# Performance work log

Measured on AMD Instinct MI355X. Metric: run time of the kernel, lower is better.

## Reference

```python
import jax, jax.numpy as jnp
import numpy as np

B, T, D = 2, 2048, 2048
NH, NKV, HD = 16, 4, 128
EPS = 1e-6
ROPE_THETA = 10000.0


def rms_norm(x, w):
    # per-head RMSNorm over the last (head_dim) axis
    var = jnp.mean(jnp.square(x), axis=-1, keepdims=True)
    return x * jax.lax.rsqrt(var + EPS) * w


def rope_sin_cos(seq_len, dim, dtype):
    inv_freq = 1.0 / (ROPE_THETA ** (jnp.arange(0, dim, 2, dtype=jnp.float32) / dim))
    t = jnp.arange(seq_len, dtype=jnp.float32)
    ang = jnp.outer(t, inv_freq)                      # [T, HD/2]
    ang = jnp.concatenate([ang, ang], axis=-1)         # [T, HD]
    return jnp.sin(ang).astype(dtype), jnp.cos(ang).astype(dtype)


def rotate_half(x):
    x1, x2 = jnp.split(x, 2, axis=-1)
    return jnp.concatenate([-x2, x1], axis=-1)


def apply_rope(x, sin, cos):
    # x: [B, T, H, HD]; sin/cos: [T, HD]
    s = sin[None, :, None, :]
    c = cos[None, :, None, :]
    return x * c + rotate_half(x) * s


def setup_inputs() -> dict:
    key = jax.random.key(0)
    ks = jax.random.split(key, 5)
    scale = 1.0 / np.sqrt(D)
    return {
        "x": jax.random.normal(ks[0], (B, T, D), jnp.float32),
        "wq": jax.random.normal(ks[1], (D, D), jnp.float32) * scale,
        "wk": jax.random.normal(ks[2], (NKV * HD, D), jnp.float32) * scale,
        "wv": jax.random.normal(ks[3], (NKV * HD, D), jnp.float32) * scale,
        "wo": jax.random.normal(ks[4], (D, D), jnp.float32) * scale,
        "q_norm_w": jnp.ones((HD,), jnp.float32),
        "k_norm_w": jnp.ones((HD,), jnp.float32),
    }


def reference(x, wq, wk, wv, wo, q_norm_w, k_norm_w):
    b, t, _ = x.shape
    q = (x @ wq.T).reshape(b, t, NH, HD)    # [B,T,NH,HD]
    k = (x @ wk.T).reshape(b, t, NKV, HD)   # [B,T,NKV,HD]
    v = (x @ wv.T).reshape(b, t, NKV, HD)

    # per-head QK RMS norm
    q = rms_norm(q, q_norm_w)
    k = rms_norm(k, k_norm_w)

    # RoPE
    sin, cos = rope_sin_cos(t, HD, x.dtype)
    q = apply_rope(q, sin, cos)
    k = apply_rope(k, sin, cos)

    # GQA: expand kv heads to match query heads
    rep = NH // NKV
    k = jnp.repeat(k, rep, axis=2)          # [B,T,NH,HD]
    v = jnp.repeat(v, rep, axis=2)

    # causal SDPA
    scale = 1.0 / np.sqrt(HD)
    scores = jnp.einsum('bqhd,bkhd->bhqk', q, k) * scale
    causal = jnp.tril(jnp.ones((t, t), bool))
    scores = jnp.where(causal[None, None], scores, jnp.finfo(scores.dtype).min)
    probs = jax.nn.softmax(scores, axis=-1)
    att = jnp.einsum('bhqk,bkhd->bqhd', probs, v).reshape(b, t, NH * HD)
    return att @ wo.T
```

## Files before the change

kernel.cpp:

```cpp
#include <hip/hip_runtime.h>
#include <hip/hip_bf16.h>

#define B_ 2
#define T_ 2048
#define D_ 2048
#define NH_ 16
#define NKV_ 4
#define HD_ 128

using bf16 = __bf16;
using bf16x8 = __attribute__((ext_vector_type(8))) __bf16;
using bf16x4 = __attribute__((ext_vector_type(4))) __bf16;
using f32x4 = __attribute__((ext_vector_type(4))) float;

__device__ __forceinline__ void gld_lds16(bf16* lds, const bf16* g) {
  __builtin_amdgcn_global_load_lds(
      (const __attribute__((address_space(1))) void*)g,
      (__attribute__((address_space(3))) void*)lds, 16, 0, 0);
}

__global__ __launch_bounds__(256) void cvt_all(const float* __restrict__ x,
                                               const float* __restrict__ wq,
                                               const float* __restrict__ wk,
                                               const float* __restrict__ wv,
                                               const float* __restrict__ wo,
                                               bf16* __restrict__ xb,
                                               bf16* __restrict__ wqkvb,
                                               bf16* __restrict__ wob) {
  const int bid = blockIdx.x;
  const float* src;
  bf16* dst;
  int base;
  if (bid < 8192)       { src = x;  dst = xb;              base = bid; }
  else if (bid < 12288) { src = wq; dst = wqkvb;           base = bid - 8192; }
  else if (bid < 13312) { src = wk; dst = wqkvb + 4194304; base = bid - 12288; }
  else if (bid < 14336) { src = wv; dst = wqkvb + 5242880; base = bid - 13312; }
  else                  { src = wo; dst = wob;             base = bid - 14336; }
  const int i = base * 256 + threadIdx.x;
  float4 v = ((const float4*)src)[i];
  bf16x4 o;
  o[0] = (bf16)v.x; o[1] = (bf16)v.y; o[2] = (bf16)v.z; o[3] = (bf16)v.w;
  ((bf16x4*)dst)[i] = o;
}

template<typename OutT>
__global__ __launch_bounds__(256) void gemm_bt(const bf16* __restrict__ A,
                                               const bf16* __restrict__ Bt,
                                               OutT* __restrict__ C,
                                               int M, int N, int K) {
  __shared__ bf16 As[3][128 * 32];
  __shared__ bf16 Bs[3][128 * 32];
  const int tid = threadIdx.x;
  const int wid = tid >> 6;
  const int lane = tid & 63;
  const int g = lane >> 4, r = lane & 15;
  const int wm = wid >> 1, wn = wid & 1;
  const int gx = gridDim.x;
  const int nwg = gx * gridDim.y;
  const int flat = blockIdx.y * gx + blockIdx.x;
  const int swz = (flat & 7) * (nwg >> 3) + (flat >> 3);
  const long bm = (long)(swz / gx) * 128, bn = (long)(swz % gx) * 128;
  f32x4 acc[4][4] = {};
  const int NT = K >> 5;

  auto stage = [&](int buf, int k0) {
    for (int c = 0; c < 2; ++c) {
      int ch = wid * 2 + c;
      int row = ch * 16 + (lane >> 2);
      int col = (lane & 3) * 8;
      gld_lds16(&As[buf][ch * 512], A + (bm + row) * K + k0 + col);
      gld_lds16(&Bs[buf][ch * 512], Bt + (bn + row) * K + k0 + col);
    }
  };

  stage(0, 0);
  stage(1, 32);
  for (int t = 0; t < NT; ++t) {
    if (t + 1 < NT)
      asm volatile("s_waitcnt vmcnt(4)" ::: "memory");
    else
      asm volatile("s_waitcnt vmcnt(0)" ::: "memory");
    __builtin_amdgcn_s_barrier();
    if (t + 2 < NT) stage((t + 2) % 3, (t + 2) * 32);
    const bf16* as = As[t % 3];
    const bf16* bs = Bs[t % 3];
    bf16x8 af[4], bfr[4];
    for (int m = 0; m < 4; ++m)
      af[m] = *(const bf16x8*)(as + (wm * 64 + m * 16 + r) * 32 + g * 8);
    for (int n = 0; n < 4; ++n)
      bfr[n] = *(const bf16x8*)(bs + (wn * 64 + n * 16 + r) * 32 + g * 8);
    for (int m = 0; m < 4; ++m)
      for (int n = 0; n < 4; ++n)
        acc[m][n] = __builtin_amdgcn_mfma_f32_16x16x32_bf16(af[m], bfr[n], acc[m][n], 0, 0, 0);
  }

  for (int m = 0; m < 4; ++m)
    for (int n = 0; n < 4; ++n)
      for (int e = 0; e < 4; ++e) {
        long row = bm + wm * 64 + m * 16 + g * 4 + e;
        long col = bn + wn * 64 + n * 16 + r;
        C[row * N + col] = (OutT)acc[m][n][e];
      }
}

__global__ __launch_bounds__(256) void prep_kv(const bf16* __restrict__ qkv,
                                               const float* __restrict__ kw,
                                               bf16* __restrict__ Kb,
                                               bf16* __restrict__ Vt) {
  __shared__ float tile[64][65];
  const int bid = blockIdx.x;
  if (bid < 4096) {
    const int lane = threadIdx.x & 63;
    const int rloc = threadIdx.x >> 6;
    const long rid = (long)bid * 4 + rloc;
    const int h = (int)(rid % NKV_);
    const long bt = rid / NKV_;
    const int t = (int)(bt % T_);
    const bf16* src = qkv + bt * 3072 + 2048 + h * HD_;
    float v0 = (float)src[lane];
    float v1 = (float)src[lane + 64];
    float ss = v0 * v0 + v1 * v1;
    for (int o = 1; o < 64; o <<= 1) ss += __shfl_xor(ss, o, 64);
    float inv = rsqrtf(ss * (1.f / HD_) + 1e-6f);
    float n0 = v0 * inv * kw[lane];
    float n1 = v1 * inv * kw[lane + 64];
    float ang = (float)t * exp2f((float)lane * (-13.287712379549449f / 64.f));
    float sv, cv;
    __sincosf(ang, &sv, &cv);
    long b = bt / T_;
    bf16* dst = Kb + ((b * NKV_ + h) * (long)T_ + t) * HD_;
    dst[lane] = (bf16)(n0 * cv - n1 * sv);
    dst[lane + 64] = (bf16)(n1 * cv + n0 * sv);
  } else {
    const int bid2 = bid - 4096;
    const int tt = bid2 & 31;
    const int by = bid2 >> 5;
    const int dd = by & 1;
    const int bkv = by >> 1;
    const long b = bkv >> 2;
    const int kv = bkv & 3;
    const int t0 = tt * 64, d0 = dd * 64;
    for (int i = 0; i < 2; ++i) {
      int row = i * 32 + (threadIdx.x >> 3);
      int c8 = (threadIdx.x & 7) * 8;
      bf16x8 v = *(const bf16x8*)&qkv[(b * T_ + t0 + row) * 3072 + 2560 + kv * HD_ + d0 + c8];
      for (int j = 0; j < 8; ++j) tile[row][c8 + j] = (float)v[j];
    }
    __syncthreads();
    for (int i = 0; i < 2; ++i) {
      int drow = i * 32 + (threadIdx.x >> 3);
      int tc8 = (threadIdx.x & 7) * 8;
      bf16x8 o;
      for (int j = 0; j < 8; ++j) o[j] = (bf16)tile[tc8 + j][drow];
      *(bf16x8*)&Vt[((b * NKV_ + kv) * (long)HD_ + d0 + drow) * T_ + t0 + tc8] = o;
    }
  }
}

__global__ __launch_bounds__(512) void flash_attn(const bf16* __restrict__ QKV,
                                                  const float* __restrict__ qw,
                                                  const bf16* __restrict__ K,
                                                  const bf16* __restrict__ V,
                                                  bf16* __restrict__ O) {
  __shared__ bf16 Ks[2][64 * 128];
  __shared__ bf16 Vs[2][128 * 64];
  __shared__ bf16 Ps[8][16 * 64];
  const int h = blockIdx.y, b = blockIdx.z;
  const int qt = b ? blockIdx.x : (gridDim.x - 1) - blockIdx.x;
  const int kv = h >> 2;
  const int tid = threadIdx.x, wid = tid >> 6, lane = tid & 63;
  const int g = lane >> 4, r = lane & 15;
  const int q0 = qt * 128;
  const int qbase = q0 + wid * 16;
  const int q = qbase + r;

  const bf16* qsrc = QKV + ((long)(b * T_ + q)) * 3072 + h * HD_;
  float ss = 0.f;
  for (int kk = 0; kk < 4; ++kk) {
    bf16x8 tq = *(const bf16x8*)(qsrc + kk * 32 + g * 8);
    for (int j = 0; j < 8; ++j) { float f = (float)tq[j]; ss += f * f; }
  }
  ss += __shfl_xor(ss, 16, 64);
  ss += __shfl_xor(ss, 32, 64);
  const float inv = rsqrtf(ss * (1.f / HD_) + 1e-6f);
  bf16x8 aq[4];
  for (int kk = 0; kk < 2; ++kk) {
    bf16x8 tlo = *(const bf16x8*)(qsrc + kk * 32 + g * 8);
    bf16x8 thi = *(const bf16x8*)(qsrc + kk * 32 + 64 + g * 8);
    bf16x8 alo, ahi;
    for (int j = 0; j < 8; ++j) {
      const int d = kk * 32 + g * 8 + j;
      float n0 = (float)tlo[j] * inv * qw[d];
      float n1 = (float)thi[j] * inv * qw[d + 64];
      float ang = (float)q * exp2f((float)d * (-13.287712379549449f / 64.f));
      float sv, cv;
      __sincosf(ang, &sv, &cv);
      alo[j] = (bf16)(n0 * cv - n1 * sv);
      ahi[j] = (bf16)(n1 * cv + n0 * sv);
    }
    aq[kk] = alo;
    aq[kk + 2] = ahi;
  }

  f32x4 oacc[8] = {};
  float m_run = -1e30f, l_run = 0.f;

  const bf16* Kbase = K + ((long)(b * NKV_ + kv)) * T_ * HD_;
  const bf16* Vbase = V + ((long)(b * NKV_ + kv)) * (long)HD_ * T_;
  const int nkt = 2 * qt + 2;

  auto stageKV = [&](int buf, int k0) {
    for (int c = 0; c < 2; ++c) {
      int ch = wid * 2 + c;
      {
        int row = ch * 4 + (lane >> 4);
        int srccol = ((lane & 15) ^ (row & 7)) * 8;
        gld_lds16(&Ks[buf][ch * 512], Kbase + (long)(k0 + row) * HD_ + srccol);
      }
      {
        int row = ch * 8 + (lane >> 3);
        int srccol = ((lane & 7) ^ (row & 7)) * 8;
        gld_lds16(&Vs[buf][ch * 512], Vbase + (long)row * T_ + k0 + srccol);
      }
    }
  };

  stageKV(0, 0);
  for (int kt = 0; kt < nkt; ++kt) {
    const int k0 = kt * 64;
    const int cur = kt & 1;
    if (kt + 1 < nkt) {
      stageKV(cur ^ 1, k0 + 64);
      asm volatile("s_waitcnt vmcnt(4)" ::: "memory");
    } else {
      asm volatile("s_waitcnt vmcnt(0)" ::: "memory");
    }
    __builtin_amdgcn_s_barrier();

    f32x4 s[4] = {};
    __builtin_amdgcn_s_setprio(1);
    for (int n = 0; n < 4; ++n)
      for (int kk = 0; kk < 4; ++kk) {
        int row = n * 16 + r;
        bf16x8 bk = *(const bf16x8*)(&Ks[cur][row * 128 + (((kk * 4 + g) ^ (row & 7)) * 8)]);
        s[n] = __builtin_amdgcn_mfma_f32_16x16x32_bf16(bk, aq[kk], s[n], 0, 0, 0);
      }
    __builtin_amdgcn_s_setprio(0);

    const float scale = 0.088388347648318447f;
    const bool domask = (k0 + 63 > qbase);
    float mx = -1e30f;
    if (domask) {
      for (int n = 0; n < 4; ++n) {
        const int km = k0 + n * 16 + g * 4;
        for (int e = 0; e < 4; ++e) {
          float v = s[n][e] * scale;
          if (km + e > q) v = -1e30f;
          s[n][e] = v;
          mx = fmaxf(mx, v);
        }
      }
    } else {
      for (int n = 0; n < 4; ++n)
        for (int e = 0; e < 4; ++e) {
          float v = s[n][e] * scale;
          s[n][e] = v;
          mx = fmaxf(mx, v);
        }
    }
    mx = fmaxf(mx, __shfl_xor(mx, 16, 64));
    mx = fmaxf(mx, __shfl_xor(mx, 32, 64));
    float mnew = fmaxf(m_run, mx);
    float alpha = __expf(m_run - mnew);
    float ls = 0.f;
    for (int n = 0; n < 4; ++n) {
      bf16x4 pb;
      for (int e = 0; e < 4; ++e) {
        float p = __expf(s[n][e] - mnew);
        ls += p;
        pb[e] = (bf16)p;
      }
      int c = n * 2 + (g >> 1);
      *(bf16x4*)(&Ps[wid][r * 64 + ((c ^ (r & 7)) * 8) + (g & 1) * 4]) = pb;
    }
    ls += __shfl_xor(ls, 16, 64);
    ls += __shfl_xor(ls, 32, 64);
    m_run = mnew;
    l_run = l_run * alpha + ls;

    float al[4];
    for (int e = 0; e < 4; ++e)
      al[e] = __shfl(alpha, (lane & 48) | (g * 4 + e), 64);
    for (int dt = 0; dt < 8; ++dt)
      for (int e = 0; e < 4; ++e) oacc[dt][e] *= al[e];

    asm volatile("s_waitcnt lgkmcnt(0)" ::: "memory");

    __builtin_amdgcn_s_setprio(1);
    for (int kk = 0; kk < 2; ++kk) {
      bf16x8 ap = *(const bf16x8*)(&Ps[wid][r * 64 + (((kk * 4 + g) ^ (r & 7)) * 8)]);
      for (int dt = 0; dt < 8; ++dt) {
        int row = dt * 16 + r;
        bf16x8 bv = *(const bf16x8*)(&Vs[cur][row * 64 + (((kk * 4 + g) ^ (row & 7)) * 8)]);
        oacc[dt] = __builtin_amdgcn_mfma_f32_16x16x32_bf16(ap, bv, oacc[dt], 0, 0, 0);
      }
    }
    __builtin_amdgcn_s_setprio(0);
    __builtin_amdgcn_s_barrier();
  }

  float li[4];
  for (int e = 0; e < 4; ++e) {
    float lv = __shfl(l_run, (lane & 48) | (g * 4 + e), 64);
    li[e] = 1.f / lv;
  }
  for (int e = 0; e < 4; ++e) {
    const int grow = q0 + wid * 16 + g * 4 + e;
    bf16* dst = O + ((long)(b * T_ + grow)) * (NH_ * HD_) + h * HD_;
    for (int dt = 0; dt < 8; ++dt)
      dst[dt * 16 + r] = (bf16)(oacc[dt][e] * li[e]);
  }
}

extern "C" void kernel_launch(void* const* d_in, const int* in_sizes, int n_in,
                              void* d_out, int out_size, void* d_ws, size_t ws_size,
                              hipStream_t stream) {
  const float* x  = (const float*)d_in[0];
  const float* wq = (const float*)d_in[1];
  const float* wk = (const float*)d_in[2];
  const float* wv = (const float*)d_in[3];
  const float* wo = (const float*)d_in[4];
  const float* qw = (const float*)d_in[5];
  const float* kw = (const float*)d_in[6];
  float* out = (float*)d_out;

  char* p = (char*)d_ws;
  bf16* xb    = (bf16*)(p);
  bf16* wqkvb = (bf16*)(p + 16777216);
  bf16* wob   = (bf16*)(p + 29360128);
  bf16* QKVr  = (bf16*)(p + 37748736);
  bf16* Kb    = (bf16*)(p + 79691776);
  bf16* Vt    = (bf16*)(p + 83886080);
  bf16* attb  = (bf16*)(p + 88080384);

  cvt_all<<<18432, 256, 0, stream>>>(x, wq, wk, wv, wo, xb, wqkvb, wob);

  gemm_bt<bf16><<<dim3(24, 32), 256, 0, stream>>>(xb, wqkvb, QKVr, 4096, 3072, 2048);

  prep_kv<<<4608, 256, 0, stream>>>(QKVr, kw, Kb, Vt);

  flash_attn<<<dim3(16, 16, 2), 512, 0, stream>>>(QKVr, qw, Kb, Vt, attb);

  gemm_bt<float><<<dim3(16, 32), 256, 0, stream>>>(attb, wob, out, 4096, 2048, 2048);
}
```

Measured before the change: 207.2 us.

## Balance causal flash attention work by splitting long query tiles across blocks

Each block now gets an equal amount of causal work. The first 8 bins process the first 17 key tiles of a long query tile. The other bins process the remainder of one long query tile plus a whole short query tile. Partial outputs of the long tiles are written as unnormalized bf16 values along with their running max and sum, and a new merge kernel combines the two pieces. This removes the tail imbalance of the causal triangle. The cost is an extra kernel launch, partial writes and reads in bf16, and reuse of the workspace region that held xb.

```diff
diff --git a/kernel.cpp b/kernel.cpp
--- a/kernel.cpp
+++ b/kernel.cpp
@@ -161,53 +161,32 @@
                                                   const float* __restrict__ qw,
                                                   const bf16* __restrict__ K,
                                                   const bf16* __restrict__ V,
-                                                  bf16* __restrict__ O) {
+                                                  bf16* __restrict__ O,
+                                                  bf16* __restrict__ OPart,
+                                                  float* __restrict__ Mst,
+                                                  float* __restrict__ Lst) {
   __shared__ bf16 Ks[2][64 * 128];
   __shared__ bf16 Vs[2][128 * 64];
   __shared__ bf16 Ps[8][16 * 64];
+  const int bin = blockIdx.x;
   const int h = blockIdx.y, b = blockIdx.z;
-  const int qt = b ? blockIdx.x : (gridDim.x - 1) - blockIdx.x;
   const int kv = h >> 2;
   const int tid = threadIdx.x, wid = tid >> 6, lane = tid & 63;
   const int g = lane >> 4, r = lane & 15;
-  const int q0 = qt * 128;
-  const int qbase = q0 + wid * 16;
-  const int q = qbase + r;
-
-  const bf16* qsrc = QKV + ((long)(b * T_ + q)) * 3072 + h * HD_;
-  float ss = 0.f;
-  for (int kk = 0; kk < 4; ++kk) {
-    bf16x8 tq = *(const bf16x8*)(qsrc + kk * 32 + g * 8);
-    for (int j = 0; j < 8; ++j) { float f = (float)tq[j]; ss += f * f; }
+
+  int segQt[2], segBeg[2], segEnd[2], nseg;
+  if (bin < 8) {
+    nseg = 1;
+    segQt[0] = 15 - bin; segBeg[0] = 0; segEnd[0] = 17;
+  } else {
+    const int i = bin - 8;
+    nseg = 2;
+    segQt[0] = 15 - i; segBeg[0] = 17; segEnd[0] = 2 * (15 - i) + 2;
+    segQt[1] = i;      segBeg[1] = 0;  segEnd[1] = 2 * i + 2;
   }
-  ss += __shfl_xor(ss, 16, 64);
-  ss += __shfl_xor(ss, 32, 64);
-  const float inv = rsqrtf(ss * (1.f / HD_) + 1e-6f);
-  bf16x8 aq[4];
-  for (int kk = 0; kk < 2; ++kk) {
-    bf16x8 tlo = *(const bf16x8*)(qsrc + kk * 32 + g * 8);
-    bf16x8 thi = *(const bf16x8*)(qsrc + kk * 32 + 64 + g * 8);
-    bf16x8 alo, ahi;
-    for (int j = 0; j < 8; ++j) {
-      const int d = kk * 32 + g * 8 + j;
-      float n0 = (float)tlo[j] * inv * qw[d];
-      float n1 = (float)thi[j] * inv * qw[d + 64];
-      float ang = (float)q * exp2f((float)d * (-13.287712379549449f / 64.f));
-      float sv, cv;
-      __sincosf(ang, &sv, &cv);
-      alo[j] = (bf16)(n0 * cv - n1 * sv);
-      ahi[j] = (bf16)(n1 * cv + n0 * sv);
-    }
-    aq[kk] = alo;
-    aq[kk + 2] = ahi;
-  }
-
-  f32x4 oacc[8] = {};
-  float m_run = -1e30f, l_run = 0.f;
 
   const bf16* Kbase = K + ((long)(b * NKV_ + kv)) * T_ * HD_;
   const bf16* Vbase = V + ((long)(b * NKV_ + kv)) * (long)HD_ * T_;
-  const int nkt = 2 * qt + 2;
 
   auto stageKV = [&](int buf, int k0) {
     for (int c = 0; c < 2; ++c) {
@@ -225,101 +204,188 @@
     }
   };
 
-  stageKV(0, 0);
-  for (int kt = 0; kt < nkt; ++kt) {
-    const int k0 = kt * 64;
-    const int cur = kt & 1;
-    if (kt + 1 < nkt) {
-      stageKV(cur ^ 1, k0 + 64);
-      asm volatile("s_waitcnt vmcnt(4)" ::: "memory");
+  stageKV(0, segBeg[0] * 64);
+  int flat = 0;
+  for (int sg = 0; sg < nseg; ++sg) {
+    const int qt = segQt[sg];
+    const int q0 = qt * 128;
+    const int qbase = q0 + wid * 16;
+    const int q = qbase + r;
+
+    const bf16* qsrc = QKV + ((long)(b * T_ + q)) * 3072 + h * HD_;
+    float ssq = 0.f;
+    for (int kk = 0; kk < 4; ++kk) {
+      bf16x8 tq = *(const bf16x8*)(qsrc + kk * 32 + g * 8);
+      for (int j = 0; j < 8; ++j) { float f = (float)tq[j]; ssq += f * f; }
+    }
+    ssq += __shfl_xor(ssq, 16, 64);
+    ssq += __shfl_xor(ssq, 32, 64);
+    const float qinv = rsqrtf(ssq * (1.f / HD_) + 1e-6f);
+    bf16x8 aq[4];
+    for (int kk = 0; kk < 2; ++kk) {
+      bf16x8 tlo = *(const bf16x8*)(qsrc + kk * 32 + g * 8);
+      bf16x8 thi = *(const bf16x8*)(qsrc + kk * 32 + 64 + g * 8);
+      bf16x8 alo, ahi;
+      for (int j = 0; j < 8; ++j) {
+        const int d = kk * 32 + g * 8 + j;
+        float n0 = (float)tlo[j] * qinv * qw[d];
+        float n1 = (float)thi[j] * qinv * qw[d + 64];
+        float ang = (float)q * exp2f((float)d * (-13.287712379549449f / 64.f));
+        float sv, cv;
+        __sincosf(ang, &sv, &cv);
+        alo[j] = (bf16)(n0 * cv - n1 * sv);
+        ahi[j] = (bf16)(n1 * cv + n0 * sv);
+      }
+      aq[kk] = alo;
+      aq[kk + 2] = ahi;
+    }
+
+    f32x4 oacc[8] = {};
+    float m_run = -1e30f, l_run = 0.f;
+
+    const int kBeg = segBeg[sg], kEnd = segEnd[sg];
+    for (int kt = kBeg; kt < kEnd; ++kt, ++flat) {
+      const int k0 = kt * 64;
+      const int cur = flat & 1;
+      int k0n = -1;
+      if (kt + 1 < kEnd) k0n = (kt + 1) * 64;
+      else if (sg + 1 < nseg) k0n = segBeg[sg + 1] * 64;
+      if (k0n >= 0) {
+        stageKV(cur ^ 1, k0n);
+        asm volatile("s_waitcnt vmcnt(4)" ::: "memory");
+      } else {
+        asm volatile("s_waitcnt vmcnt(0)" ::: "memory");
+      }
+      __builtin_amdgcn_s_barrier();
+
+      f32x4 s[4] = {};
+      __builtin_amdgcn_s_setprio(1);
+      for (int n = 0; n < 4; ++n)
+        for (int kk = 0; kk < 4; ++kk) {
+          int row = n * 16 + r;
+          bf16x8 bk = *(const bf16x8*)(&Ks[cur][row * 128 + (((kk * 4 + g) ^ (row & 7)) * 8)]);
+          s[n] = __builtin_amdgcn_mfma_f32_16x16x32_bf16(bk, aq[kk], s[n], 0, 0, 0);
+        }
+      __builtin_amdgcn_s_setprio(0);
+
+      const float scale = 0.088388347648318447f;
+      const bool domask = (k0 + 63 > qbase);
+      float mx = -1e30f;
+      if (domask) {
+        for (int n = 0; n < 4; ++n) {
+          const int km = k0 + n * 16 + g * 4;
+          for (int e = 0; e < 4; ++e) {
+            float v = s[n][e] * scale;
+            if (km + e > q) v = -1e30f;
+            s[n][e] = v;
+            mx = fmaxf(mx, v);
+          }
+        }
+      } else {
+        for (int n = 0; n < 4; ++n)
+          for (int e = 0; e < 4; ++e) {
+            float v = s[n][e] * scale;
+            s[n][e] = v;
+            mx = fmaxf(mx, v);
+          }
+      }
+      mx = fmaxf(mx, __shfl_xor(mx, 16, 64));
+      mx = fmaxf(mx, __shfl_xor(mx, 32, 64));
+      float mnew = fmaxf(m_run, mx);
+      float alpha = __expf(m_run - mnew);
+      const float mden = fmaxf(mnew, -1e28f);
+      float ls = 0.f;
+      for (int n = 0; n < 4; ++n) {
+        bf16x4 pb;
+        for (int e = 0; e < 4; ++e) {
+          float p = __expf(s[n][e] - mden);
+          ls += p;
+          pb[e] = (bf16)p;
+        }
+        int c = n * 2 + (g >> 1);
+        *(bf16x4*)(&Ps[wid][r * 64 + ((c ^ (r & 7)) * 8) + (g & 1) * 4]) = pb;
+      }
+      ls += __shfl_xor(ls, 16, 64);
+      ls += __shfl_xor(ls, 32, 64);
+      m_run = mnew;
+      l_run = l_run * alpha + ls;
+
+      float al[4];
+      for (int e = 0; e < 4; ++e)
+        al[e] = __shfl(alpha, (lane & 48) | (g * 4 + e), 64);
+      for (int dt = 0; dt < 8; ++dt)
+        for (int e = 0; e < 4; ++e) oacc[dt][e] *= al[e];
+
+      asm volatile("s_waitcnt lgkmcnt(0)" ::: "memory");
+
+      __builtin_amdgcn_s_setprio(1);
+      for (int kk = 0; kk < 2; ++kk) {
+        bf16x8 ap = *(const bf16x8*)(&Ps[wid][r * 64 + (((kk * 4 + g) ^ (r & 7)) * 8)]);
+        for (int dt = 0; dt < 8; ++dt) {
+          int row = dt * 16 + r;
+          bf16x8 bv = *(const bf16x8*)(&Vs[cur][row * 64 + (((kk * 4 + g) ^ (row & 7)) * 8)]);
+          oacc[dt] = __builtin_amdgcn_mfma_f32_16x16x32_bf16(ap, bv, oacc[dt], 0, 0, 0);
+        }
+      }
+      __builtin_amdgcn_s_setprio(0);
+      __builtin_amdgcn_s_barrier();
+    }
+
+    if (qt >= 8) {
+      const int piece = (bin >= 8 && sg == 0) ? 1 : 0;
+      const int pid = (((b * 16 + h) * 8) + (qt - 8)) * 2 + piece;
+      bf16* dst0 = OPart + (long)pid * 16384;
+      for (int e = 0; e < 4; ++e) {
+        const int rowl = wid * 16 + g * 4 + e;
+        bf16* dst = dst0 + rowl * 128;
+        for (int dt = 0; dt < 8; ++dt) dst[dt * 16 + r] = (bf16)oacc[dt][e];
+      }
+      if (g == 0) {
+        Mst[pid * 128 + wid * 16 + r] = m_run;
+        Lst[pid * 128 + wid * 16 + r] = l_run;
+      }
     } else {
-      asm volatile("s_waitcnt vmcnt(0)" ::: "memory");
-    }
-    __builtin_amdgcn_s_barrier();
-
-    f32x4 s[4] = {};
-    __builtin_amdgcn_s_setprio(1);
-    for (int n = 0; n < 4; ++n)
-      for (int kk = 0; kk < 4; ++kk) {
-        int row = n * 16 + r;
-        bf16x8 bk = *(const bf16x8*)(&Ks[cur][row * 128 + (((kk * 4 + g) ^ (row & 7)) * 8)]);
-        s[n] = __builtin_amdgcn_mfma_f32_16x16x32_bf16(bk, aq[kk], s[n], 0, 0, 0);
-      }
-    __builtin_amdgcn_s_setprio(0);
-
-    const float scale = 0.088388347648318447f;
-    const bool domask = (k0 + 63 > qbase);
-    float mx = -1e30f;
-    if (domask) {
-      for (int n = 0; n < 4; ++n) {
-        const int km = k0 + n * 16 + g * 4;
-        for (int e = 0; e < 4; ++e) {
-          float v = s[n][e] * scale;
-          if (km + e > q) v = -1e30f;
-          s[n][e] = v;
-          mx = fmaxf(mx, v);
-        }
-      }
-    } else {
-      for (int n = 0; n < 4; ++n)
-        for (int e = 0; e < 4; ++e) {
-          float v = s[n][e] * scale;
-          s[n][e] = v;
-          mx = fmaxf(mx, v);
-        }
-    }
-    mx = fmaxf(mx, __shfl_xor(mx, 16, 64));
-    mx = fmaxf(mx, __shfl_xor(mx, 32, 64));
-    float mnew = fmaxf(m_run, mx);
-    float alpha = __expf(m_run - mnew);
-    float ls = 0.f;
-    for (int n = 0; n < 4; ++n) {
-      bf16x4 pb;
+      float li[4];
       for (int e = 0; e < 4; ++e) {
-        float p = __expf(s[n][e] - mnew);
-        ls += p;
-        pb[e] = (bf16)p;
-      }
-      int c = n * 2 + (g >> 1);
-      *(bf16x4*)(&Ps[wid][r * 64 + ((c ^ (r & 7)) * 8) + (g & 1) * 4]) = pb;
-    }
-    ls += __shfl_xor(ls, 16, 64);
-    ls += __shfl_xor(ls, 32, 64);
-    m_run = mnew;
-    l_run = l_run * alpha + ls;
-
-    float al[4];
-    for (int e = 0; e < 4; ++e)
-      al[e] = __shfl(alpha, (lane & 48) | (g * 4 + e), 64);
-    for (int dt = 0; dt < 8; ++dt)
-      for (int e = 0; e < 4; ++e) oacc[dt][e] *= al[e];
-
-    asm volatile("s_waitcnt lgkmcnt(0)" ::: "memory");
-
-    __builtin_amdgcn_s_setprio(1);
-    for (int kk = 0; kk < 2; ++kk) {
-      bf16x8 ap = *(const bf16x8*)(&Ps[wid][r * 64 + (((kk * 4 + g) ^ (r & 7)) * 8)]);
-      for (int dt = 0; dt < 8; ++dt) {
-        int row = dt * 16 + r;
-        bf16x8 bv = *(const bf16x8*)(&Vs[cur][row * 64 + (((kk * 4 + g) ^ (row & 7)) * 8)]);
-        oacc[dt] = __builtin_amdgcn_mfma_f32_16x16x32_bf16(ap, bv, oacc[dt], 0, 0, 0);
-      }
-    }
-    __builtin_amdgcn_s_setprio(0);
-    __builtin_amdgcn_s_barrier();
+        float lv = __shfl(l_run, (lane & 48) | (g * 4 + e), 64);
+        li[e] = 1.f / lv;
+      }
+      for (int e = 0; e < 4; ++e) {
+        const int grow = q0 + wid * 16 + g * 4 + e;
+        bf16* dst = O + ((long)(b * T_ + grow)) * (NH_ * HD_) + h * HD_;
+        for (int dt = 0; dt < 8; ++dt)
+          dst[dt * 16 + r] = (bf16)(oacc[dt][e] * li[e]);
+      }
+    }
   }
-
-  float li[4];
-  for (int e = 0; e < 4; ++e) {
-    float lv = __shfl(l_run, (lane & 48) | (g * 4 + e), 64);
-    li[e] = 1.f / lv;
-  }
-  for (int e = 0; e < 4; ++e) {
-    const int grow = q0 + wid * 16 + g * 4 + e;
-    bf16* dst = O + ((long)(b * T_ + grow)) * (NH_ * HD_) + h * HD_;
-    for (int dt = 0; dt < 8; ++dt)
-      dst[dt * 16 + r] = (bf16)(oacc[dt][e] * li[e]);
-  }
+}
+
+__global__ __launch_bounds__(256) void merge_o(const bf16* __restrict__ OPart,
+                                               const float* __restrict__ Mst,
+                                               const float* __restrict__ Lst,
+                                               bf16* __restrict__ attb) {
+  const int bid = blockIdx.x;
+  const int qi = bid >> 3;
+  const int row = (bid & 7) * 16 + (threadIdx.x >> 4);
+  const int d8 = (threadIdx.x & 15) * 8;
+  const int qt = 8 + (qi & 7);
+  const int hb = qi >> 3;
+  const int h = hb & 15;
+  const int b = hb >> 4;
+  const int pid0 = qi * 2;
+  const bf16* o0p = OPart + (long)pid0 * 16384 + row * 128 + d8;
+  const bf16* o1p = OPart + (long)(pid0 + 1) * 16384 + row * 128 + d8;
+  bf16x8 o0 = *(const bf16x8*)o0p;
+  bf16x8 o1 = *(const bf16x8*)o1p;
+  const float m0 = Mst[pid0 * 128 + row], l0 = Lst[pid0 * 128 + row];
+  const float m1 = Mst[(pid0 + 1) * 128 + row], l1 = Lst[(pid0 + 1) * 128 + row];
+  const float M = fmaxf(m0, m1);
+  const float w0 = __expf(m0 - M), w1 = __expf(m1 - M);
+  const float inv = 1.f / (l0 * w0 + l1 * w1);
+  bf16x8 res;
+  for (int j = 0; j < 8; ++j)
+    res[j] = (bf16)(((float)o0[j] * w0 + (float)o1[j] * w1) * inv);
+  *(bf16x8*)&attb[((long)(b * T_ + qt * 128 + row)) * 2048 + h * 128 + d8] = res;
 }
 
 extern "C" void kernel_launch(void* const* d_in, const int* in_sizes, int n_in,
@@ -342,6 +408,9 @@
   bf16* Kb    = (bf16*)(p + 79691776);
   bf16* Vt    = (bf16*)(p + 83886080);
   bf16* attb  = (bf16*)(p + 88080384);
+  bf16*  OPart = (bf16*)(p);
+  float* Mst   = (float*)(p + 16777216);
+  float* Lst   = (float*)(p + 17039360);
 
   cvt_all<<<18432, 256, 0, stream>>>(x, wq, wk, wv, wo, xb, wqkvb, wob);
 
@@ -349,7 +418,9 @@
 
   prep_kv<<<4608, 256, 0, stream>>>(QKVr, kw, Kb, Vt);
 
-  flash_attn<<<dim3(16, 16, 2), 512, 0, stream>>>(QKVr, qw, Kb, Vt, attb);
+  flash_attn<<<dim3(16, 16, 2), 512, 0, stream>>>(QKVr, qw, Kb, Vt, attb,
+                                                  OPart, Mst, Lst);
+  merge_o<<<2048, 256, 0, stream>>>(OPart, Mst, Lst, attb);
 
   gemm_bt<float><<<dim3(16, 32), 256, 0, stream>>>(attb, wob, out, 4096, 2048, 2048);
 }
```

Result: slower. 219.7 us (+6.0%).

## Split flash-attention key tiles across warp pairs with 64-row query blocks and merge

Applied to the files above, without the earlier changes.

Query tiles shrink from 128 to 64 rows and the grid doubles. Each pair of warps now splits every 64-key tile into two 32-key halves, keeping separate online-softmax states that are merged through shared memory at the end. The K/V double buffer becomes a single buffer, with the next tile's load issued only after the trailing barrier, which cuts LDS use to 40 KB so more blocks can be resident. The aim is more parallelism and better load balance across CUs, at the cost of losing the overlap between loads and compute, an extra merge step, and a clamp on the exp reference for fully masked rows.

```diff
diff --git a/kernel.cpp b/kernel.cpp
--- a/kernel.cpp
+++ b/kernel.cpp
@@ -162,27 +162,36 @@
                                                   const bf16* __restrict__ K,
                                                   const bf16* __restrict__ V,
                                                   bf16* __restrict__ O) {
-  __shared__ bf16 Ks[2][64 * 128];
-  __shared__ bf16 Vs[2][128 * 64];
-  __shared__ bf16 Ps[8][16 * 64];
+  __shared__ char smem[40960];
+  bf16* Ks = (bf16*)smem;
+  bf16* Vs = (bf16*)(smem + 16384);
+  bf16* Ps = (bf16*)(smem + 32768);
+  float* mergeO = (float*)smem;
+  float* mergeML = (float*)(smem + 32768);
+
   const int h = blockIdx.y, b = blockIdx.z;
-  const int qt = b ? blockIdx.x : (gridDim.x - 1) - blockIdx.x;
+  const int x = blockIdx.x;
+  const int y8 = (h >> 3) & 1;
+  const int qt = b ? (y8 ? 31 - (x ^ 1) : (x ^ 1)) : (y8 ? x : 31 - x);
   const int kv = h >> 2;
   const int tid = threadIdx.x, wid = tid >> 6, lane = tid & 63;
   const int g = lane >> 4, r = lane & 15;
-  const int q0 = qt * 128;
-  const int qbase = q0 + wid * 16;
+  const int f = wid >> 1;
+  const int gr = wid & 1;
+  const int ko = gr * 32;
+  const int q0 = qt * 64;
+  const int qbase = q0 + f * 16;
   const int q = qbase + r;
 
   const bf16* qsrc = QKV + ((long)(b * T_ + q)) * 3072 + h * HD_;
-  float ss = 0.f;
+  float ssq = 0.f;
   for (int kk = 0; kk < 4; ++kk) {
     bf16x8 tq = *(const bf16x8*)(qsrc + kk * 32 + g * 8);
-    for (int j = 0; j < 8; ++j) { float f = (float)tq[j]; ss += f * f; }
-  }
-  ss += __shfl_xor(ss, 16, 64);
-  ss += __shfl_xor(ss, 32, 64);
-  const float inv = rsqrtf(ss * (1.f / HD_) + 1e-6f);
+    for (int j = 0; j < 8; ++j) { float ff = (float)tq[j]; ssq += ff * ff; }
+  }
+  ssq += __shfl_xor(ssq, 16, 64);
+  ssq += __shfl_xor(ssq, 32, 64);
+  const float qinv = rsqrtf(ssq * (1.f / HD_) + 1e-6f);
   bf16x8 aq[4];
   for (int kk = 0; kk < 2; ++kk) {
     bf16x8 tlo = *(const bf16x8*)(qsrc + kk * 32 + g * 8);
@@ -190,8 +199,8 @@
     bf16x8 alo, ahi;
     for (int j = 0; j < 8; ++j) {
       const int d = kk * 32 + g * 8 + j;
-      float n0 = (float)tlo[j] * inv * qw[d];
-      float n1 = (float)thi[j] * inv * qw[d + 64];
+      float n0 = (float)tlo[j] * qinv * qw[d];
+      float n1 = (float)thi[j] * qinv * qw[d + 64];
       float ang = (float)q * exp2f((float)d * (-13.287712379549449f / 64.f));
       float sv, cv;
       __sincosf(ang, &sv, &cv);
@@ -207,52 +216,48 @@
 
   const bf16* Kbase = K + ((long)(b * NKV_ + kv)) * T_ * HD_;
   const bf16* Vbase = V + ((long)(b * NKV_ + kv)) * (long)HD_ * T_;
-  const int nkt = 2 * qt + 2;
-
-  auto stageKV = [&](int buf, int k0) {
+  const int nkt = qt + 1;
+
+  auto stageKV = [&](int k0) {
     for (int c = 0; c < 2; ++c) {
       int ch = wid * 2 + c;
       {
         int row = ch * 4 + (lane >> 4);
         int srccol = ((lane & 15) ^ (row & 7)) * 8;
-        gld_lds16(&Ks[buf][ch * 512], Kbase + (long)(k0 + row) * HD_ + srccol);
+        gld_lds16(&Ks[ch * 512], Kbase + (long)(k0 + row) * HD_ + srccol);
       }
       {
         int row = ch * 8 + (lane >> 3);
         int srccol = ((lane & 7) ^ (row & 7)) * 8;
-        gld_lds16(&Vs[buf][ch * 512], Vbase + (long)row * T_ + k0 + srccol);
+        gld_lds16(&Vs[ch * 512], Vbase + (long)row * T_ + k0 + srccol);
       }
     }
   };
 
-  stageKV(0, 0);
+  const float scale = 0.088388347648318447f;
+  bf16* myPs = Ps + wid * 512;
+
+  stageKV(0);
   for (int kt = 0; kt < nkt; ++kt) {
     const int k0 = kt * 64;
-    const int cur = kt & 1;
-    if (kt + 1 < nkt) {
-      stageKV(cur ^ 1, k0 + 64);
-      asm volatile("s_waitcnt vmcnt(4)" ::: "memory");
-    } else {
-      asm volatile("s_waitcnt vmcnt(0)" ::: "memory");
-    }
+    asm volatile("s_waitcnt vmcnt(0)" ::: "memory");
     __builtin_amdgcn_s_barrier();
 
-    f32x4 s[4] = {};
+    f32x4 s[2] = {};
     __builtin_amdgcn_s_setprio(1);
-    for (int n = 0; n < 4; ++n)
+    for (int n = 0; n < 2; ++n)
       for (int kk = 0; kk < 4; ++kk) {
-        int row = n * 16 + r;
-        bf16x8 bk = *(const bf16x8*)(&Ks[cur][row * 128 + (((kk * 4 + g) ^ (row & 7)) * 8)]);
+        int row = ko + n * 16 + r;
+        bf16x8 bk = *(const bf16x8*)(&Ks[row * 128 + (((kk * 4 + g) ^ (row & 7)) * 8)]);
         s[n] = __builtin_amdgcn_mfma_f32_16x16x32_bf16(bk, aq[kk], s[n], 0, 0, 0);
       }
     __builtin_amdgcn_s_setprio(0);
 
-    const float scale = 0.088388347648318447f;
-    const bool domask = (k0 + 63 > qbase);
+    const bool domask = (k0 + ko + 31 > qbase);
     float mx = -1e30f;
     if (domask) {
-      for (int n = 0; n < 4; ++n) {
-        const int km = k0 + n * 16 + g * 4;
+      for (int n = 0; n < 2; ++n) {
+        const int km = k0 + ko + n * 16 + g * 4;
         for (int e = 0; e < 4; ++e) {
           float v = s[n][e] * scale;
           if (km + e > q) v = -1e30f;
@@ -261,7 +266,7 @@
         }
       }
     } else {
-      for (int n = 0; n < 4; ++n)
+      for (int n = 0; n < 2; ++n)
         for (int e = 0; e < 4; ++e) {
           float v = s[n][e] * scale;
           s[n][e] = v;
@@ -272,16 +277,17 @@
     mx = fmaxf(mx, __shfl_xor(mx, 32, 64));
     float mnew = fmaxf(m_run, mx);
     float alpha = __expf(m_run - mnew);
+    const float mden = fmaxf(mnew, -1e28f);
     float ls = 0.f;
-    for (int n = 0; n < 4; ++n) {
+    for (int n = 0; n < 2; ++n) {
       bf16x4 pb;
       for (int e = 0; e < 4; ++e) {
-        float p = __expf(s[n][e] - mnew);
+        float p = __expf(s[n][e] - mden);
         ls += p;
         pb[e] = (bf16)p;
       }
       int c = n * 2 + (g >> 1);
-      *(bf16x4*)(&Ps[wid][r * 64 + ((c ^ (r & 7)) * 8) + (g & 1) * 4]) = pb;
+      *(bf16x4*)(&myPs[r * 32 + ((c ^ (r & 3)) * 8) + (g & 1) * 4]) = pb;
     }
     ls += __shfl_xor(ls, 16, 64);
     ls += __shfl_xor(ls, 32, 64);
@@ -297,28 +303,53 @@
     asm volatile("s_waitcnt lgkmcnt(0)" ::: "memory");
 
     __builtin_amdgcn_s_setprio(1);
-    for (int kk = 0; kk < 2; ++kk) {
-      bf16x8 ap = *(const bf16x8*)(&Ps[wid][r * 64 + (((kk * 4 + g) ^ (r & 7)) * 8)]);
+    {
+      bf16x8 ap = *(const bf16x8*)(&myPs[r * 32 + ((g ^ (r & 3)) * 8)]);
       for (int dt = 0; dt < 8; ++dt) {
         int row = dt * 16 + r;
-        bf16x8 bv = *(const bf16x8*)(&Vs[cur][row * 64 + (((kk * 4 + g) ^ (row & 7)) * 8)]);
+        bf16x8 bv = *(const bf16x8*)(&Vs[row * 64 + (((gr * 4 + g) ^ (row & 7)) * 8)]);
         oacc[dt] = __builtin_amdgcn_mfma_f32_16x16x32_bf16(ap, bv, oacc[dt], 0, 0, 0);
       }
     }
     __builtin_amdgcn_s_setprio(0);
     __builtin_amdgcn_s_barrier();
-  }
-
-  float li[4];
-  for (int e = 0; e < 4; ++e) {
-    float lv = __shfl(l_run, (lane & 48) | (g * 4 + e), 64);
-    li[e] = 1.f / lv;
-  }
-  for (int e = 0; e < 4; ++e) {
-    const int grow = q0 + wid * 16 + g * 4 + e;
-    bf16* dst = O + ((long)(b * T_ + grow)) * (NH_ * HD_) + h * HD_;
-    for (int dt = 0; dt < 8; ++dt)
-      dst[dt * 16 + r] = (bf16)(oacc[dt][e] * li[e]);
+    if (kt + 1 < nkt) stageKV(k0 + 64);
+  }
+
+  if (gr == 1) {
+    float* mo = mergeO + f * 2048;
+    for (int e = 0; e < 4; ++e)
+      for (int dt = 0; dt < 8; ++dt)
+        mo[(g * 4 + e) * 128 + dt * 16 + r] = oacc[dt][e];
+    if (g == 0) {
+      mergeML[f * 32 + r] = m_run;
+      mergeML[f * 32 + 16 + r] = l_run;
+    }
+  }
+  __syncthreads();
+  if (gr == 0) {
+    const float* mo = mergeO + f * 2048;
+    const float m1 = mergeML[f * 32 + r];
+    const float l1 = mergeML[f * 32 + 16 + r];
+    const float M = fmaxf(m_run, m1);
+    const float w0 = __expf(m_run - M);
+    const float w1 = __expf(m1 - M);
+    const float lt = l_run * w0 + l1 * w1;
+    float W0[4], W1[4], LI[4];
+    for (int e = 0; e < 4; ++e) {
+      const int src = (lane & 48) | (g * 4 + e);
+      W0[e] = __shfl(w0, src, 64);
+      W1[e] = __shfl(w1, src, 64);
+      LI[e] = 1.f / __shfl(lt, src, 64);
+    }
+    for (int e = 0; e < 4; ++e) {
+      const int grow = qbase + g * 4 + e;
+      bf16* dst = O + ((long)(b * T_ + grow)) * (NH_ * HD_) + h * HD_;
+      for (int dt = 0; dt < 8; ++dt) {
+        float o1 = mo[(g * 4 + e) * 128 + dt * 16 + r];
+        dst[dt * 16 + r] = (bf16)((oacc[dt][e] * W0[e] + o1 * W1[e]) * LI[e]);
+      }
+    }
   }
 }
 
@@ -349,7 +380,7 @@
 
   prep_kv<<<4608, 256, 0, stream>>>(QKVr, kw, Kb, Vt);
 
-  flash_attn<<<dim3(16, 16, 2), 512, 0, stream>>>(QKVr, qw, Kb, Vt, attb);
+  flash_attn<<<dim3(32, 16, 2), 512, 0, stream>>>(QKVr, qw, Kb, Vt, attb);
 
   gemm_bt<float><<<dim3(16, 32), 256, 0, stream>>>(attb, wob, out, 4096, 2048, 2048);
 }
```

Measured after the change: 237.0 us. 14.4% more time.

## Switch flash attention to 32x32x16 MFMA with register-resident P and 4 waves

Applied to the files above, without the earlier changes.

Rewrites the attention inner loop to use 32x32x16 bf16 MFMA tiles, with each wave owning 32 query rows, and halves the block to 256 threads. Softmax probabilities now stay in registers and are rearranged through a cross-half lane shuffle, so the shared-memory P buffer and its LDS round-trip go away. The per-row alpha and l broadcasts become lane-local, and output stores are vectorized. The cost is higher register pressure from the 16-wide accumulators and fewer waves per block for hiding latency.

```diff
diff --git a/kernel.cpp b/kernel.cpp
--- a/kernel.cpp
+++ b/kernel.cpp
@@ -12,6 +12,8 @@
 using bf16x8 = __attribute__((ext_vector_type(8))) __bf16;
 using bf16x4 = __attribute__((ext_vector_type(4))) __bf16;
 using f32x4 = __attribute__((ext_vector_type(4))) float;
+using f32x16 = __attribute__((ext_vector_type(16))) float;
+using u32x4 = __attribute__((ext_vector_type(4))) unsigned int;
 
 __device__ __forceinline__ void gld_lds16(bf16* lds, const bf16* g) {
   __builtin_amdgcn_global_load_lds(
@@ -157,52 +159,54 @@
   }
 }
 
-__global__ __launch_bounds__(512) void flash_attn(const bf16* __restrict__ QKV,
+__global__ __launch_bounds__(256) void flash_attn(const bf16* __restrict__ QKV,
                                                   const float* __restrict__ qw,
                                                   const bf16* __restrict__ K,
                                                   const bf16* __restrict__ V,
                                                   bf16* __restrict__ O) {
   __shared__ bf16 Ks[2][64 * 128];
   __shared__ bf16 Vs[2][128 * 64];
-  __shared__ bf16 Ps[8][16 * 64];
   const int h = blockIdx.y, b = blockIdx.z;
   const int qt = b ? blockIdx.x : (gridDim.x - 1) - blockIdx.x;
   const int kv = h >> 2;
   const int tid = threadIdx.x, wid = tid >> 6, lane = tid & 63;
-  const int g = lane >> 4, r = lane & 15;
+  const int ql = lane & 31, hi = lane >> 5;
   const int q0 = qt * 128;
-  const int qbase = q0 + wid * 16;
-  const int q = qbase + r;
-
-  const bf16* qsrc = QKV + ((long)(b * T_ + q)) * 3072 + h * HD_;
+  const int qbase = q0 + wid * 32;
+  const int qrow = qbase + ql;
+
+  const bf16* qsrc = QKV + ((long)(b * T_ + qrow)) * 3072 + h * HD_;
   float ss = 0.f;
-  for (int kk = 0; kk < 4; ++kk) {
-    bf16x8 tq = *(const bf16x8*)(qsrc + kk * 32 + g * 8);
+#pragma unroll
+  for (int t = 0; t < 8; ++t) {
+    bf16x8 tq = *(const bf16x8*)(qsrc + t * 16 + hi * 8);
+#pragma unroll
     for (int j = 0; j < 8; ++j) { float f = (float)tq[j]; ss += f * f; }
   }
-  ss += __shfl_xor(ss, 16, 64);
   ss += __shfl_xor(ss, 32, 64);
   const float inv = rsqrtf(ss * (1.f / HD_) + 1e-6f);
-  bf16x8 aq[4];
-  for (int kk = 0; kk < 2; ++kk) {
-    bf16x8 tlo = *(const bf16x8*)(qsrc + kk * 32 + g * 8);
-    bf16x8 thi = *(const bf16x8*)(qsrc + kk * 32 + 64 + g * 8);
+  bf16x8 aq[8];
+#pragma unroll
+  for (int t = 0; t < 4; ++t) {
+    bf16x8 tlo = *(const bf16x8*)(qsrc + t * 16 + hi * 8);
+    bf16x8 thi = *(const bf16x8*)(qsrc + (t + 4) * 16 + hi * 8);
     bf16x8 alo, ahi;
+#pragma unroll
     for (int j = 0; j < 8; ++j) {
-      const int d = kk * 32 + g * 8 + j;
+      const int d = t * 16 + hi * 8 + j;
       float n0 = (float)tlo[j] * inv * qw[d];
       float n1 = (float)thi[j] * inv * qw[d + 64];
-      float ang = (float)q * exp2f((float)d * (-13.287712379549449f / 64.f));
+      float ang = (float)qrow * exp2f((float)d * (-13.287712379549449f / 64.f));
       float sv, cv;
       __sincosf(ang, &sv, &cv);
       alo[j] = (bf16)(n0 * cv - n1 * sv);
       ahi[j] = (bf16)(n1 * cv + n0 * sv);
     }
-    aq[kk] = alo;
-    aq[kk + 2] = ahi;
-  }
-
-  f32x4 oacc[8] = {};
+    aq[t] = alo;
+    aq[t + 4] = ahi;
+  }
+
+  f32x16 oacc[4] = {};
   float m_run = -1e30f, l_run = 0.f;
 
   const bf16* Kbase = K + ((long)(b * NKV_ + kv)) * T_ * HD_;
@@ -210,8 +214,9 @@
   const int nkt = 2 * qt + 2;
 
   auto stageKV = [&](int buf, int k0) {
-    for (int c = 0; c < 2; ++c) {
-      int ch = wid * 2 + c;
+#pragma unroll
+    for (int c = 0; c < 4; ++c) {
+      int ch = wid * 4 + c;
       {
         int row = ch * 4 + (lane >> 4);
         int srccol = ((lane & 15) ^ (row & 7)) * 8;
@@ -224,6 +229,8 @@
       }
     }
   };
+
+  const float scale = 0.088388347648318447f;
 
   stageKV(0, 0);
   for (int kt = 0; kt < nkt; ++kt) {
@@ -231,95 +238,101 @@
     const int cur = kt & 1;
     if (kt + 1 < nkt) {
       stageKV(cur ^ 1, k0 + 64);
-      asm volatile("s_waitcnt vmcnt(4)" ::: "memory");
+      asm volatile("s_waitcnt vmcnt(8)" ::: "memory");
     } else {
       asm volatile("s_waitcnt vmcnt(0)" ::: "memory");
     }
     __builtin_amdgcn_s_barrier();
 
-    f32x4 s[4] = {};
+    f32x16 s[2] = {};
     __builtin_amdgcn_s_setprio(1);
-    for (int n = 0; n < 4; ++n)
-      for (int kk = 0; kk < 4; ++kk) {
-        int row = n * 16 + r;
-        bf16x8 bk = *(const bf16x8*)(&Ks[cur][row * 128 + (((kk * 4 + g) ^ (row & 7)) * 8)]);
-        s[n] = __builtin_amdgcn_mfma_f32_16x16x32_bf16(bk, aq[kk], s[n], 0, 0, 0);
-      }
+#pragma unroll
+    for (int kc = 0; kc < 2; ++kc) {
+      const int row = kc * 32 + ql;
+#pragma unroll
+      for (int t = 0; t < 8; ++t) {
+        bf16x8 bk = *(const bf16x8*)(&Ks[cur][row * 128 + (((2 * t + hi) ^ (row & 7)) * 8)]);
+        s[kc] = __builtin_amdgcn_mfma_f32_32x32x16_bf16(bk, aq[t], s[kc], 0, 0, 0);
+      }
+    }
     __builtin_amdgcn_s_setprio(0);
 
-    const float scale = 0.088388347648318447f;
     const bool domask = (k0 + 63 > qbase);
     float mx = -1e30f;
-    if (domask) {
-      for (int n = 0; n < 4; ++n) {
-        const int km = k0 + n * 16 + g * 4;
-        for (int e = 0; e < 4; ++e) {
-          float v = s[n][e] * scale;
-          if (km + e > q) v = -1e30f;
-          s[n][e] = v;
-          mx = fmaxf(mx, v);
+#pragma unroll
+    for (int kc = 0; kc < 2; ++kc)
+#pragma unroll
+      for (int r = 0; r < 16; ++r) {
+        float v = s[kc][r] * scale;
+        if (domask) {
+          int kg = k0 + kc * 32 + (r & 3) + 8 * (r >> 2) + 4 * hi;
+          if (kg > qrow) v = -1e30f;
         }
-      }
-    } else {
-      for (int n = 0; n < 4; ++n)
-        for (int e = 0; e < 4; ++e) {
-          float v = s[n][e] * scale;
-          s[n][e] = v;
-          mx = fmaxf(mx, v);
-        }
-    }
-    mx = fmaxf(mx, __shfl_xor(mx, 16, 64));
+        s[kc][r] = v;
+        mx = fmaxf(mx, v);
+      }
     mx = fmaxf(mx, __shfl_xor(mx, 32, 64));
-    float mnew = fmaxf(m_run, mx);
-    float alpha = __expf(m_run - mnew);
+    const float mnew = fmaxf(m_run, mx);
+    const float alpha = __expf(m_run - mnew);
     float ls = 0.f;
-    for (int n = 0; n < 4; ++n) {
-      bf16x4 pb;
-      for (int e = 0; e < 4; ++e) {
-        float p = __expf(s[n][e] - mnew);
-        ls += p;
-        pb[e] = (bf16)p;
-      }
-      int c = n * 2 + (g >> 1);
-      *(bf16x4*)(&Ps[wid][r * 64 + ((c ^ (r & 7)) * 8) + (g & 1) * 4]) = pb;
-    }
-    ls += __shfl_xor(ls, 16, 64);
+    unsigned int w[2][8];
+#pragma unroll
+    for (int kc = 0; kc < 2; ++kc)
+#pragma unroll
+      for (int i = 0; i < 8; ++i) {
+        float p0 = __expf(s[kc][2 * i] - mnew);
+        float p1 = __expf(s[kc][2 * i + 1] - mnew);
+        ls += p0 + p1;
+        unsigned short b0 = __builtin_bit_cast(unsigned short, (bf16)p0);
+        unsigned short b1 = __builtin_bit_cast(unsigned short, (bf16)p1);
+        w[kc][i] = ((unsigned int)b1 << 16) | (unsigned int)b0;
+      }
     ls += __shfl_xor(ls, 32, 64);
     m_run = mnew;
     l_run = l_run * alpha + ls;
-
-    float al[4];
-    for (int e = 0; e < 4; ++e)
-      al[e] = __shfl(alpha, (lane & 48) | (g * 4 + e), 64);
-    for (int dt = 0; dt < 8; ++dt)
-      for (int e = 0; e < 4; ++e) oacc[dt][e] *= al[e];
-
-    asm volatile("s_waitcnt lgkmcnt(0)" ::: "memory");
+#pragma unroll
+    for (int dt = 0; dt < 4; ++dt)
+#pragma unroll
+      for (int r = 0; r < 16; ++r) oacc[dt][r] *= alpha;
+
+    unsigned int xw[2][8];
+#pragma unroll
+    for (int kc = 0; kc < 2; ++kc)
+#pragma unroll
+      for (int i = 0; i < 8; ++i) xw[kc][i] = __shfl_xor(w[kc][i], 32, 64);
 
     __builtin_amdgcn_s_setprio(1);
-    for (int kk = 0; kk < 2; ++kk) {
-      bf16x8 ap = *(const bf16x8*)(&Ps[wid][r * 64 + (((kk * 4 + g) ^ (r & 7)) * 8)]);
-      for (int dt = 0; dt < 8; ++dt) {
-        int row = dt * 16 + r;
-        bf16x8 bv = *(const bf16x8*)(&Vs[cur][row * 64 + (((kk * 4 + g) ^ (row & 7)) * 8)]);
-        oacc[dt] = __builtin_amdgcn_mfma_f32_16x16x32_bf16(ap, bv, oacc[dt], 0, 0, 0);
+#pragma unroll
+    for (int ks = 0; ks < 4; ++ks) {
+      const int kcs = ks >> 1, o = (ks & 1) * 4;
+      unsigned int b0 = hi ? xw[kcs][o + 2] : w[kcs][o + 0];
+      unsigned int b1 = hi ? xw[kcs][o + 3] : w[kcs][o + 1];
+      unsigned int b2 = hi ? w[kcs][o + 2] : xw[kcs][o + 0];
+      unsigned int b3 = hi ? w[kcs][o + 3] : xw[kcs][o + 1];
+      u32x4 pw = {b0, b1, b2, b3};
+      bf16x8 pb = __builtin_bit_cast(bf16x8, pw);
+#pragma unroll
+      for (int dt = 0; dt < 4; ++dt) {
+        const int row = dt * 32 + ql;
+        bf16x8 av = *(const bf16x8*)(&Vs[cur][row * 64 + (((2 * ks + hi) ^ (row & 7)) * 8)]);
+        oacc[dt] = __builtin_amdgcn_mfma_f32_32x32x16_bf16(av, pb, oacc[dt], 0, 0, 0);
       }
     }
     __builtin_amdgcn_s_setprio(0);
     __builtin_amdgcn_s_barrier();
   }
 
-  float li[4];
-  for (int e = 0; e < 4; ++e) {
-    float lv = __shfl(l_run, (lane & 48) | (g * 4 + e), 64);
-    li[e] = 1.f / lv;
-  }
-  for (int e = 0; e < 4; ++e) {
-    const int grow = q0 + wid * 16 + g * 4 + e;
-    bf16* dst = O + ((long)(b * T_ + grow)) * (NH_ * HD_) + h * HD_;
-    for (int dt = 0; dt < 8; ++dt)
-      dst[dt * 16 + r] = (bf16)(oacc[dt][e] * li[e]);
-  }
+  const float linv = 1.f / l_run;
+  bf16* dst = O + ((long)(b * T_ + qrow)) * (NH_ * HD_) + h * HD_;
+#pragma unroll
+  for (int dt = 0; dt < 4; ++dt)
+#pragma unroll
+    for (int rr = 0; rr < 4; ++rr) {
+      bf16x4 o4;
+#pragma unroll
+      for (int e = 0; e < 4; ++e) o4[e] = (bf16)(oacc[dt][rr * 4 + e] * linv);
+      *(bf16x4*)(dst + dt * 32 + rr * 8 + hi * 4) = o4;
+    }
 }
 
 extern "C" void kernel_launch(void* const* d_in, const int* in_sizes, int n_in,
@@ -349,7 +362,7 @@
 
   prep_kv<<<4608, 256, 0, stream>>>(QKVr, kw, Kb, Vt);
 
-  flash_attn<<<dim3(16, 16, 2), 512, 0, stream>>>(QKVr, qw, Kb, Vt, attb);
+  flash_attn<<<dim3(16, 16, 2), 256, 0, stream>>>(QKVr, qw, Kb, Vt, attb);
 
   gemm_bt<float><<<dim3(16, 32), 256, 0, stream>>>(attb, wob, out, 4096, 2048, 2048);
 }
```

After: 274.3 us. +32.4%, slower.
